# Kernel optimization log

Measured on AMD Instinct MI355X. Metric: run time of the kernel, lower is better.

Reference implementation:

```python
import jax, jax.numpy as jnp
import numpy as np

Q_MAX = 127.0  # 8-bit, narrow range [-127, 127] (pytorch-quantization default)


def fake_quant(x, amax):
    """Fake quantization with clipped-STE semantics (matches pytorch-quantization).

    amax may be a scalar (per-tensor) or broadcastable (per-channel). Treated as
    a constant (stop_gradient'd by caller where appropriate).
    """
    amax = jnp.maximum(amax, 1e-12)
    scale = amax / Q_MAX
    xq = jnp.round(jnp.clip(x / scale, -Q_MAX, Q_MAX)) * scale
    xc = jnp.clip(x, -amax, amax)  # identity grad inside range, zero outside
    return xc + jax.lax.stop_gradient(xq - xc)


def quant_conv1x1(x, w, b):
    """QuantConv2d with 1x1 kernel: fake-quant input (per-tensor dynamic max amax)
    and weight (per-output-channel max amax), then conv + bias.
    x: [B,C,H,W], w: [O,C], b: [O]
    """
    a_amax = jax.lax.stop_gradient(jnp.max(jnp.abs(x)))
    xq = fake_quant(x, a_amax)
    w_amax = jax.lax.stop_gradient(jnp.max(jnp.abs(w), axis=1, keepdims=True))
    wq = fake_quant(w, w_amax)
    y = jnp.einsum('bchw,oc->bohw', xq, wq)
    return y + b[None, :, None, None]


def setup_inputs() -> dict:
    key = jax.random.key(0)
    k1, k2, k3, k4 = jax.random.split(key, 4)
    B, C, Cr, H, W = 64, 32, 8, 128, 128
    x = jax.random.normal(k1, (B, C, H, W), dtype=jnp.float32)
    identity = jax.random.normal(k2, (B, C, H, W), dtype=jnp.float32)
    w_reduce = jax.random.normal(k3, (Cr, C), dtype=jnp.float32) * 0.1
    b_reduce = jnp.zeros((Cr,), dtype=jnp.float32)
    w_expand = jax.random.normal(k4, (C, Cr), dtype=jnp.float32) * 0.1
    b_expand = jnp.zeros((C,), dtype=jnp.float32)
    return {"x": x, "identity": identity,
            "w_reduce": w_reduce, "b_reduce": b_reduce,
            "w_expand": w_expand, "b_expand": b_expand}


def reference(x, identity, w_reduce, b_reduce, w_expand, b_expand):
    h = quant_conv1x1(x, w_reduce, b_reduce)      # [B,8,H,W]
    h = h * jax.nn.sigmoid(h)                     # SiLU
    g = quant_conv1x1(h, w_expand, b_expand)      # [B,32,H,W]
    return identity * jax.nn.sigmoid(g)
```

## Files before the change

### kernel.cpp

```cpp
#include <hip/hip_runtime.h>
#include <math.h>

#define QMAX 127.0f
#define CIN 32
#define CR 8
#define HW 16384
#define BATCH 64
#define NPIX (BATCH*HW)
#define NQUAD (NPIX/4)
#define NX (BATCH*CIN*HW)


__device__ __forceinline__ float fq(float v, float inv_scale, float scale) {
    return rintf(fminf(fmaxf(v * inv_scale, -QMAX), QMAX)) * scale;
}
__device__ __forceinline__ float sigmoidf_(float v) {
    return 1.0f / (1.0f + __expf(-v));
}

__global__ __launch_bounds__(256) void k0_prep(const float* __restrict__ wr,
                                               const float* __restrict__ we,
                                               float* __restrict__ wsf,
                                               unsigned int* __restrict__ wsu) {
    int t = threadIdx.x;
    if (t < 2) wsu[t] = 0u;
    __shared__ float amr[CR], ame[CIN];
    if (t < CR) {
        float m = 0.f;
        for (int c = 0; c < CIN; c++) m = fmaxf(m, fabsf(wr[t * CIN + c]));
        amr[t] = fmaxf(m, 1e-12f);
    }
    if (t >= 64 && t < 64 + CIN) {
        int r = t - 64;
        float m = 0.f;
        for (int c = 0; c < CR; c++) m = fmaxf(m, fabsf(we[r * CR + c]));
        ame[r] = fmaxf(m, 1e-12f);
    }
    __syncthreads();
    {
        int r = t >> 5;
        float amax = amr[r];
        wsf[8 + t] = fq(wr[t], QMAX / amax, amax * (1.f / QMAX));
    }
    {
        int r = t >> 3;
        float amax = ame[r];
        wsf[264 + t] = fq(we[t], QMAX / amax, amax * (1.f / QMAX));
    }
}

__global__ __launch_bounds__(256) void k1_xmax(const float4* __restrict__ x4,
                                               unsigned int* __restrict__ wsu) {
    float m = 0.f;
    int stride = gridDim.x * 256;
    for (int i = blockIdx.x * 256 + threadIdx.x; i < NX / 4; i += stride) {
        float4 v = x4[i];
        m = fmaxf(m, fmaxf(fmaxf(fabsf(v.x), fabsf(v.y)), fmaxf(fabsf(v.z), fabsf(v.w))));
    }
#pragma unroll
    for (int off = 32; off > 0; off >>= 1) m = fmaxf(m, __shfl_xor(m, off, 64));
    __shared__ float red[4];
    int t = threadIdx.x;
    if ((t & 63) == 0) red[t >> 6] = m;
    __syncthreads();
    if (t == 0) {
        m = fmaxf(fmaxf(red[0], red[1]), fmaxf(red[2], red[3]));
        atomicMax(&wsu[0], __float_as_uint(m));
    }
}

__global__ __launch_bounds__(256) void k2_hmax(const float* __restrict__ x,
                                               const float* __restrict__ br,
                                               const float* __restrict__ wsf,
                                               const unsigned int* __restrict__ wsu,
                                               unsigned int* __restrict__ hmax) {
    __shared__ float wq[CR * CIN];
    __shared__ float bsh[CR];
    int t = threadIdx.x;
    wq[t] = wsf[8 + t];
    if (t < CR) bsh[t] = br[t];
    __syncthreads();
    float a_amax = fmaxf(__uint_as_float(wsu[0]), 1e-12f);
    float scale = a_amax * (1.f / QMAX), inv_scale = QMAX / a_amax;
    int tid = blockIdx.x * 256 + t;
    int b = tid >> 12;
    int hw = (tid & 4095) << 2;
    const float* xb = x + (size_t)b * CIN * HW + hw;
    float hacc[CR][4];
#pragma unroll
    for (int o = 0; o < CR; o++)
#pragma unroll
        for (int v = 0; v < 4; v++) hacc[o][v] = 0.f;
#pragma unroll
    for (int c = 0; c < CIN; c++) {
        float4 xv = *(const float4*)(xb + (size_t)c * HW);
        float q0 = fq(xv.x, inv_scale, scale), q1 = fq(xv.y, inv_scale, scale);
        float q2 = fq(xv.z, inv_scale, scale), q3 = fq(xv.w, inv_scale, scale);
#pragma unroll
        for (int o = 0; o < CR; o++) {
            float w = wq[o * CIN + c];
            hacc[o][0] += q0 * w; hacc[o][1] += q1 * w;
            hacc[o][2] += q2 * w; hacc[o][3] += q3 * w;
        }
    }
    float m = 0.f;
#pragma unroll
    for (int o = 0; o < CR; o++) {
        float bb = bsh[o];
#pragma unroll
        for (int v = 0; v < 4; v++) {
            float h = hacc[o][v] + bb;
            h = h * sigmoidf_(h);
            m = fmaxf(m, fabsf(h));
        }
    }
#pragma unroll
    for (int off = 32; off > 0; off >>= 1) m = fmaxf(m, __shfl_xor(m, off, 64));
    __shared__ float red[4];
    if ((t & 63) == 0) red[t >> 6] = m;
    __syncthreads();
    if (t == 0) {
        m = fmaxf(fmaxf(red[0], red[1]), fmaxf(red[2], red[3]));
        atomicMax(hmax, __float_as_uint(m));
    }
}

__global__ __launch_bounds__(256) void k3_out(const float* __restrict__ x,
                                              const float* __restrict__ identity,
                                              const float* __restrict__ br,
                                              const float* __restrict__ be,
                                              const float* __restrict__ wsf,
                                              const unsigned int* __restrict__ wsu,
                                              float* __restrict__ out) {
    __shared__ float wqr[CR * CIN], wqe[CIN * CR], bsh[CR], besh[CIN];
    int t = threadIdx.x;
    wqr[t] = wsf[8 + t];
    wqe[t] = wsf[264 + t];
    if (t < CR) bsh[t] = br[t];
    if (t < CIN) besh[t] = be[t];
    __syncthreads();
    float a_amax = fmaxf(__uint_as_float(wsu[0]), 1e-12f);
    float ascale = a_amax * (1.f / QMAX), ainv = QMAX / a_amax;
    float h_amax = fmaxf(__uint_as_float(wsu[1]), 1e-12f);
    float hscale = h_amax * (1.f / QMAX), hinv = QMAX / h_amax;
    int tid = blockIdx.x * 256 + t;
    int b = tid >> 12;
    int hw = (tid & 4095) << 2;
    size_t base = (size_t)b * CIN * HW + hw;
    const float* xb = x + base;

    float hq[CR][4];
    {
        float hacc[CR][4];
#pragma unroll
        for (int o = 0; o < CR; o++)
#pragma unroll
            for (int v = 0; v < 4; v++) hacc[o][v] = 0.f;
#pragma unroll
        for (int c = 0; c < CIN; c++) {
            float4 xv = *(const float4*)(xb + (size_t)c * HW);
            float q0 = fq(xv.x, ainv, ascale), q1 = fq(xv.y, ainv, ascale);
            float q2 = fq(xv.z, ainv, ascale), q3 = fq(xv.w, ainv, ascale);
#pragma unroll
            for (int o = 0; o < CR; o++) {
                float w = wqr[o * CIN + c];
                hacc[o][0] += q0 * w; hacc[o][1] += q1 * w;
                hacc[o][2] += q2 * w; hacc[o][3] += q3 * w;
            }
        }
#pragma unroll
        for (int o = 0; o < CR; o++) {
            float bb = bsh[o];
#pragma unroll
            for (int v = 0; v < 4; v++) {
                float h = hacc[o][v] + bb;
                h = h * sigmoidf_(h);
                hq[o][v] = fq(h, hinv, hscale);
            }
        }
    }
#pragma unroll 4
    for (int o2 = 0; o2 < CIN; o2++) {
        float g0 = besh[o2], g1 = g0, g2 = g0, g3 = g0;
#pragma unroll
        for (int cr = 0; cr < CR; cr++) {
            float w = wqe[o2 * CR + cr];
            g0 += hq[cr][0] * w; g1 += hq[cr][1] * w;
            g2 += hq[cr][2] * w; g3 += hq[cr][3] * w;
        }
        float4 idv = *(const float4*)(identity + base + (size_t)o2 * HW);
        float4 ov;
        ov.x = idv.x * sigmoidf_(g0);
        ov.y = idv.y * sigmoidf_(g1);
        ov.z = idv.z * sigmoidf_(g2);
        ov.w = idv.w * sigmoidf_(g3);
        *(float4*)(out + base + (size_t)o2 * HW) = ov;
    }
}

extern "C" void kernel_launch(void* const* d_in, const int* in_sizes, int n_in,
                              void* d_out, int out_size, void* d_ws, size_t ws_size,
                              hipStream_t stream) {
    const float* x        = (const float*)d_in[0];
    const float* identity = (const float*)d_in[1];
    const float* wr       = (const float*)d_in[2];
    const float* br       = (const float*)d_in[3];
    const float* we       = (const float*)d_in[4];
    const float* be       = (const float*)d_in[5];
    float* out            = (float*)d_out;
    float* wsf            = (float*)d_ws;
    unsigned int* wsu     = (unsigned int*)d_ws;

    hipLaunchKernelGGL(k0_prep, dim3(1), dim3(256), 0, stream, wr, we, wsf, wsu);
    hipLaunchKernelGGL(k1_xmax, dim3(2048), dim3(256), 0, stream, (const float4*)x, wsu);
    hipLaunchKernelGGL(k2_hmax, dim3(NQUAD / 256), dim3(256), 0, stream, x, br, wsf, wsu, &wsu[1]);
    hipLaunchKernelGGL(k3_out,  dim3(NQUAD / 256), dim3(256), 0, stream, x, identity, br, be, wsf, wsu, out);
}
```

Before: 395.9 us.

## Materialize SiLU activations in workspace to avoid re-reading input in output kernel

The hmax kernel now stores the post-SiLU reduced activations to a workspace buffer. The output kernel reads these instead of recomputing the first conv from x, and splits output channels across two grid rows. Weight quantization is folded into the consumer kernels, removing the separate prep launch, and the x-max loop is unrolled to a fixed count. The new path depends on workspace size and falls back to the recompute kernel otherwise.

```diff
diff --git a/kernel.cpp b/kernel.cpp
--- a/kernel.cpp
+++ b/kernel.cpp
@@ -10,6 +10,8 @@
 #define NQUAD (NPIX/4)
 #define NX (BATCH*CIN*HW)
 
+#define H_OFF 64
+#define WS_NEEDED ((size_t)(H_OFF + (size_t)NPIX * CR) * 4)
 
 __device__ __forceinline__ float fq(float v, float inv_scale, float scale) {
     return rintf(fminf(fmaxf(v * inv_scale, -QMAX), QMAX)) * scale;
@@ -18,43 +20,13 @@
     return 1.0f / (1.0f + __expf(-v));
 }
 
-__global__ __launch_bounds__(256) void k0_prep(const float* __restrict__ wr,
-                                               const float* __restrict__ we,
-                                               float* __restrict__ wsf,
-                                               unsigned int* __restrict__ wsu) {
-    int t = threadIdx.x;
-    if (t < 2) wsu[t] = 0u;
-    __shared__ float amr[CR], ame[CIN];
-    if (t < CR) {
-        float m = 0.f;
-        for (int c = 0; c < CIN; c++) m = fmaxf(m, fabsf(wr[t * CIN + c]));
-        amr[t] = fmaxf(m, 1e-12f);
-    }
-    if (t >= 64 && t < 64 + CIN) {
-        int r = t - 64;
-        float m = 0.f;
-        for (int c = 0; c < CR; c++) m = fmaxf(m, fabsf(we[r * CR + c]));
-        ame[r] = fmaxf(m, 1e-12f);
-    }
-    __syncthreads();
-    {
-        int r = t >> 5;
-        float amax = amr[r];
-        wsf[8 + t] = fq(wr[t], QMAX / amax, amax * (1.f / QMAX));
-    }
-    {
-        int r = t >> 3;
-        float amax = ame[r];
-        wsf[264 + t] = fq(we[t], QMAX / amax, amax * (1.f / QMAX));
-    }
-}
-
 __global__ __launch_bounds__(256) void k1_xmax(const float4* __restrict__ x4,
                                                unsigned int* __restrict__ wsu) {
+    int idx = blockIdx.x * 256 + threadIdx.x;
     float m = 0.f;
-    int stride = gridDim.x * 256;
-    for (int i = blockIdx.x * 256 + threadIdx.x; i < NX / 4; i += stride) {
-        float4 v = x4[i];
+#pragma unroll
+    for (int i = 0; i < 16; i++) {
+        float4 v = x4[idx + i * 524288];
         m = fmaxf(m, fmaxf(fmaxf(fabsf(v.x), fabsf(v.y)), fmaxf(fabsf(v.z), fabsf(v.w))));
     }
 #pragma unroll
@@ -70,15 +42,24 @@
 }
 
 __global__ __launch_bounds__(256) void k2_hmax(const float* __restrict__ x,
+                                               const float* __restrict__ wr,
                                                const float* __restrict__ br,
-                                               const float* __restrict__ wsf,
                                                const unsigned int* __restrict__ wsu,
-                                               unsigned int* __restrict__ hmax) {
-    __shared__ float wq[CR * CIN];
-    __shared__ float bsh[CR];
-    int t = threadIdx.x;
-    wq[t] = wsf[8 + t];
-    if (t < CR) bsh[t] = br[t];
+                                               unsigned int* __restrict__ hmax,
+                                               float* __restrict__ hbuf) {
+    __shared__ float wq[CR * CIN], bsh[CR], amr[CR];
+    int t = threadIdx.x;
+    if (t < CR) {
+        float mm = 0.f;
+        for (int c = 0; c < CIN; c++) mm = fmaxf(mm, fabsf(wr[t * CIN + c]));
+        amr[t] = fmaxf(mm, 1e-12f);
+        bsh[t] = br[t];
+    }
+    __syncthreads();
+    {
+        float amax = amr[t >> 5];
+        wq[t] = fq(wr[t], QMAX / amax, amax * (1.f / QMAX));
+    }
     __syncthreads();
     float a_amax = fmaxf(__uint_as_float(wsu[0]), 1e-12f);
     float scale = a_amax * (1.f / QMAX), inv_scale = QMAX / a_amax;
@@ -107,12 +88,16 @@
 #pragma unroll
     for (int o = 0; o < CR; o++) {
         float bb = bsh[o];
+        float4 hv;
+        float* hp = (float*)&hv;
 #pragma unroll
         for (int v = 0; v < 4; v++) {
             float h = hacc[o][v] + bb;
             h = h * sigmoidf_(h);
+            hp[v] = h;
             m = fmaxf(m, fabsf(h));
         }
+        if (hbuf) *(float4*)(hbuf + ((size_t)(b * CR + o)) * HW + hw) = hv;
     }
 #pragma unroll
     for (int off = 32; off > 0; off >>= 1) m = fmaxf(m, __shfl_xor(m, off, 64));
@@ -125,19 +110,95 @@
     }
 }
 
-__global__ __launch_bounds__(256) void k3_out(const float* __restrict__ x,
+__global__ __launch_bounds__(256) void k3_out(const float* __restrict__ hbuf,
                                               const float* __restrict__ identity,
-                                              const float* __restrict__ br,
+                                              const float* __restrict__ we,
                                               const float* __restrict__ be,
-                                              const float* __restrict__ wsf,
                                               const unsigned int* __restrict__ wsu,
                                               float* __restrict__ out) {
-    __shared__ float wqr[CR * CIN], wqe[CIN * CR], bsh[CR], besh[CIN];
-    int t = threadIdx.x;
-    wqr[t] = wsf[8 + t];
-    wqe[t] = wsf[264 + t];
-    if (t < CR) bsh[t] = br[t];
-    if (t < CIN) besh[t] = be[t];
+    const int y = blockIdx.y;
+    __shared__ float wqe[16 * CR], besh[16], ame[16];
+    int t = threadIdx.x;
+    if (t < 16) {
+        int r = 16 * y + t;
+        float mm = 0.f;
+        for (int c = 0; c < CR; c++) mm = fmaxf(mm, fabsf(we[r * CR + c]));
+        ame[t] = fmaxf(mm, 1e-12f);
+        besh[t] = be[r];
+    }
+    __syncthreads();
+    if (t < 128) {
+        int r16 = t >> 3;
+        float amax = ame[r16];
+        wqe[t] = fq(we[(16 * y + r16) * CR + (t & 7)], QMAX / amax, amax * (1.f / QMAX));
+    }
+    __syncthreads();
+    float h_amax = fmaxf(__uint_as_float(wsu[1]), 1e-12f);
+    float hscale = h_amax * (1.f / QMAX), hinv = QMAX / h_amax;
+    int tid = blockIdx.x * 256 + t;
+    int b = tid >> 12;
+    int hw = (tid & 4095) << 2;
+    size_t base = (size_t)b * CIN * HW + hw;
+
+    float hq[CR][4];
+#pragma unroll
+    for (int cr = 0; cr < CR; cr++) {
+        float4 hv = *(const float4*)(hbuf + ((size_t)(b * CR + cr)) * HW + hw);
+        hq[cr][0] = fq(hv.x, hinv, hscale);
+        hq[cr][1] = fq(hv.y, hinv, hscale);
+        hq[cr][2] = fq(hv.z, hinv, hscale);
+        hq[cr][3] = fq(hv.w, hinv, hscale);
+    }
+#pragma unroll 4
+    for (int o = 0; o < 16; o++) {
+        float g0 = besh[o], g1 = g0, g2 = g0, g3 = g0;
+#pragma unroll
+        for (int cr = 0; cr < CR; cr++) {
+            float w = wqe[o * CR + cr];
+            g0 += hq[cr][0] * w; g1 += hq[cr][1] * w;
+            g2 += hq[cr][2] * w; g3 += hq[cr][3] * w;
+        }
+        size_t off = base + (size_t)(16 * y + o) * HW;
+        float4 idv = *(const float4*)(identity + off);
+        float4 ov;
+        ov.x = idv.x * sigmoidf_(g0);
+        ov.y = idv.y * sigmoidf_(g1);
+        ov.z = idv.z * sigmoidf_(g2);
+        ov.w = idv.w * sigmoidf_(g3);
+        *(float4*)(out + off) = ov;
+    }
+}
+
+__global__ __launch_bounds__(256) void k3_out_rc(const float* __restrict__ x,
+                                                 const float* __restrict__ identity,
+                                                 const float* __restrict__ wr,
+                                                 const float* __restrict__ br,
+                                                 const float* __restrict__ we,
+                                                 const float* __restrict__ be,
+                                                 const unsigned int* __restrict__ wsu,
+                                                 float* __restrict__ out) {
+    __shared__ float wqr[CR * CIN], wqe[CIN * CR], bsh[CR], besh[CIN], amr[CR], ame[CIN];
+    int t = threadIdx.x;
+    if (t < CR) {
+        float mm = 0.f;
+        for (int c = 0; c < CIN; c++) mm = fmaxf(mm, fabsf(wr[t * CIN + c]));
+        amr[t] = fmaxf(mm, 1e-12f);
+        bsh[t] = br[t];
+    }
+    if (t >= 64 && t < 64 + CIN) {
+        int r = t - 64;
+        float mm = 0.f;
+        for (int c = 0; c < CR; c++) mm = fmaxf(mm, fabsf(we[r * CR + c]));
+        ame[r] = fmaxf(mm, 1e-12f);
+        besh[r] = be[r];
+    }
+    __syncthreads();
+    {
+        float amax = amr[t >> 5];
+        wqr[t] = fq(wr[t], QMAX / amax, amax * (1.f / QMAX));
+        float amax2 = ame[t >> 3];
+        wqe[t] = fq(we[t], QMAX / amax2, amax2 * (1.f / QMAX));
+    }
     __syncthreads();
     float a_amax = fmaxf(__uint_as_float(wsu[0]), 1e-12f);
     float ascale = a_amax * (1.f / QMAX), ainv = QMAX / a_amax;
@@ -148,7 +209,6 @@
     int hw = (tid & 4095) << 2;
     size_t base = (size_t)b * CIN * HW + hw;
     const float* xb = x + base;
-
     float hq[CR][4];
     {
         float hacc[CR][4];
@@ -188,13 +248,14 @@
             g0 += hq[cr][0] * w; g1 += hq[cr][1] * w;
             g2 += hq[cr][2] * w; g3 += hq[cr][3] * w;
         }
-        float4 idv = *(const float4*)(identity + base + (size_t)o2 * HW);
+        size_t off = base + (size_t)o2 * HW;
+        float4 idv = *(const float4*)(identity + off);
         float4 ov;
         ov.x = idv.x * sigmoidf_(g0);
         ov.y = idv.y * sigmoidf_(g1);
         ov.z = idv.z * sigmoidf_(g2);
         ov.w = idv.w * sigmoidf_(g3);
-        *(float4*)(out + base + (size_t)o2 * HW) = ov;
+        *(float4*)(out + off) = ov;
     }
 }
 
@@ -210,9 +271,18 @@
     float* out            = (float*)d_out;
     float* wsf            = (float*)d_ws;
     unsigned int* wsu     = (unsigned int*)d_ws;
-
-    hipLaunchKernelGGL(k0_prep, dim3(1), dim3(256), 0, stream, wr, we, wsf, wsu);
+    const bool big_ws     = (ws_size >= WS_NEEDED);
+    float* hbuf           = big_ws ? (wsf + H_OFF) : nullptr;
+
+    hipMemsetAsync(d_ws, 0, 16, stream);
     hipLaunchKernelGGL(k1_xmax, dim3(2048), dim3(256), 0, stream, (const float4*)x, wsu);
-    hipLaunchKernelGGL(k2_hmax, dim3(NQUAD / 256), dim3(256), 0, stream, x, br, wsf, wsu, &wsu[1]);
-    hipLaunchKernelGGL(k3_out,  dim3(NQUAD / 256), dim3(256), 0, stream, x, identity, br, be, wsf, wsu, out);
-}
+    hipLaunchKernelGGL(k2_hmax, dim3(NQUAD / 256), dim3(256), 0, stream,
+                       x, wr, br, wsu, &wsu[1], hbuf);
+    if (big_ws) {
+        hipLaunchKernelGGL(k3_out, dim3(NQUAD / 256, 2), dim3(256), 0, stream,
+                           hbuf, identity, we, be, wsu, out);
+    } else {
+        hipLaunchKernelGGL(k3_out_rc, dim3(NQUAD / 256), dim3(256), 0, stream,
+                           x, identity, wr, br, we, be, wsu, out);
+    }
+}
```

After: 382.9 us. -3.3%, faster.
